# Optimization experiments

Measured on AMD Instinct MI355X. Metric: run time of the kernel, lower is better.

Reference implementation:

```python
import jax, jax.numpy as jnp
import numpy as np

B, TQ, TI, TT = 8, 256, 256, 256
H, NH, F, E = 1024, 16, 4096, 8
HD = H // NH
EPS = 1e-5


def _ln(x, g, b):
    m = x.mean(-1, keepdims=True)
    v = ((x - m) ** 2).mean(-1, keepdims=True)
    return (x - m) / jnp.sqrt(v + EPS) * g + b


def _mha(q, k, v, in_w, in_b, out_w, out_b):
    # torch nn.MultiheadAttention: packed in_proj [3H,H], out_proj [H,H]
    wq, wk, wv = jnp.split(in_w, 3, axis=0)
    bq, bk, bv = jnp.split(in_b, 3, axis=0)
    Bq, Tq, _ = q.shape
    Tk = k.shape[1]
    qh = (q @ wq.T + bq).reshape(Bq, Tq, NH, HD)
    kh = (k @ wk.T + bk).reshape(Bq, Tk, NH, HD)
    vh = (v @ wv.T + bv).reshape(Bq, Tk, NH, HD)
    scores = jnp.einsum('bqhd,bkhd->bhqk', qh, kh) / jnp.sqrt(jnp.float32(HD))
    attn = jax.nn.softmax(scores, axis=-1)
    out = jnp.einsum('bhqk,bkhd->bqhd', attn, vh).reshape(Bq, Tq, H)
    return out @ out_w.T + out_b


def _moe(x, w1, b1, w2, b2, probs):
    # dense all-expert FFN: GELU(x W1 + b1) W2 + b2, mixed by router probs
    h = jax.nn.gelu(jnp.einsum('bth,ehf->btef', x, w1) + b1, approximate=False)
    o = jnp.einsum('btef,efh->bteh', h, w2) + b2
    return (o * probs[..., None]).sum(axis=-2)


def setup_inputs() -> dict:
    key = jax.random.key(0)
    ks = jax.random.split(key, 24)
    s = 0.02
    d = {}
    d['query_tokens'] = jax.random.normal(ks[0], (B, TQ, H), jnp.float32)
    d['image_tokens'] = jax.random.normal(ks[1], (B, TI, H), jnp.float32)
    d['text_context'] = jax.random.normal(ks[2], (B, TT, H), jnp.float32)
    d['sa_in_w'] = jax.random.normal(ks[3], (3 * H, H), jnp.float32) * s
    d['sa_in_b'] = jnp.zeros((3 * H,), jnp.float32)
    d['sa_out_w'] = jax.random.normal(ks[4], (H, H), jnp.float32) * s
    d['sa_out_b'] = jnp.zeros((H,), jnp.float32)
    d['ca_in_w'] = jax.random.normal(ks[5], (3 * H, H), jnp.float32) * s
    d['ca_in_b'] = jnp.zeros((3 * H,), jnp.float32)
    d['ca_out_w'] = jax.random.normal(ks[6], (H, H), jnp.float32) * s
    d['ca_out_b'] = jnp.zeros((H,), jnp.float32)
    d['img_gate_w'] = jax.random.normal(ks[7], (E, 2 * H), jnp.float32) * s
    d['img_gate_b'] = jnp.zeros((E,), jnp.float32)
    d['txt_gate_w'] = jax.random.normal(ks[8], (E, 2 * H), jnp.float32) * s
    d['txt_gate_b'] = jnp.zeros((E,), jnp.float32)
    d['lnq_g'] = jnp.ones((H,), jnp.float32)
    d['lnq_b'] = jnp.zeros((H,), jnp.float32)
    d['lnc_g'] = jnp.ones((H,), jnp.float32)
    d['lnc_b'] = jnp.zeros((H,), jnp.float32)
    d['lnf_g'] = jnp.ones((H,), jnp.float32)
    d['lnf_b'] = jnp.zeros((H,), jnp.float32)
    d['ew1'] = jax.random.normal(ks[9], (E, H, F), jnp.float32) * s
    d['eb1'] = jnp.zeros((E, F), jnp.float32)
    d['ew2'] = jax.random.normal(ks[10], (E, F, H), jnp.float32) * s
    d['eb2'] = jnp.zeros((E, H), jnp.float32)
    return d


def reference(query_tokens, image_tokens, text_context,
              sa_in_w, sa_in_b, sa_out_w, sa_out_b,
              ca_in_w, ca_in_b, ca_out_w, ca_out_b,
              img_gate_w, img_gate_b, txt_gate_w, txt_gate_b,
              lnq_g, lnq_b, lnc_g, lnc_b, lnf_g, lnf_b,
              ew1, eb1, ew2, eb2):
    # self-attention on query stream (dropout is identity in eval)
    q_norm = _ln(query_tokens, lnq_g, lnq_b)
    query_tokens = query_tokens + _mha(q_norm, q_norm, q_norm, sa_in_w, sa_in_b, sa_out_w, sa_out_b)
    # cross-attention query -> image tokens
    cross_norm = _ln(query_tokens, lnc_g, lnc_b)
    query_tokens = query_tokens + _mha(cross_norm, image_tokens, image_tokens, ca_in_w, ca_in_b, ca_out_w, ca_out_b)
    # gating contexts
    image_ctx = image_tokens.mean(axis=1, keepdims=True)   # [B,1,H]
    text_ctx = text_context.mean(axis=1, keepdims=True)    # [B,1,H]
    img_gate_in = jnp.concatenate([image_tokens, jnp.broadcast_to(text_ctx, image_tokens.shape)], axis=-1)
    txt_gate_in = jnp.concatenate([query_tokens, jnp.broadcast_to(image_ctx, query_tokens.shape)], axis=-1)
    temp = jnp.maximum(jnp.float32(1.0), 0.001)  # router temperature buffer = 1.0
    image_probs = jax.nn.softmax((img_gate_in @ img_gate_w.T + img_gate_b) / temp, axis=-1)
    text_probs = jax.nn.softmax((txt_gate_in @ txt_gate_w.T + txt_gate_b) / temp, axis=-1)
    # dense MoE (ep_group is None -> all experts evaluated, mixed by full softmax)
    q_ffn = _ln(query_tokens, lnf_g, lnf_b)
    query_tokens = query_tokens + _moe(q_ffn, ew1, eb1, ew2, eb2, text_probs)
    image_tokens = image_tokens + _moe(image_tokens, ew1, eb1, ew2, eb2, image_probs)
    return query_tokens, image_tokens
```

## Files before the change

kernel.cpp:

```cpp
#include <hip/hip_runtime.h>
#include <math.h>

typedef unsigned short u16;
typedef __bf16 bf16x8 __attribute__((ext_vector_type(8)));
typedef float  f32x4  __attribute__((ext_vector_type(4)));
typedef unsigned short u16x8 __attribute__((ext_vector_type(8)));
typedef unsigned short u16x4 __attribute__((ext_vector_type(4)));

union B8 { u16x8 u; bf16x8 b; };

__device__ __forceinline__ u16 f2bf(float x) {
  unsigned int u = __float_as_uint(x);
  unsigned int r = (u + 0x7fffu + ((u >> 16) & 1u)) >> 16;
  return (u16)r;
}
__device__ __forceinline__ float bf2f(u16 h) {
  return __uint_as_float(((unsigned int)h) << 16);
}

__device__ __forceinline__ void gload16(const void* g, void* l) {
  __builtin_amdgcn_global_load_lds(
      (const __attribute__((address_space(1))) unsigned int*)g,
      (__attribute__((address_space(3))) unsigned int*)l, 16, 0, 0);
}

__global__ __launch_bounds__(256) void cast_kernel(const float* __restrict__ in,
                                                   u16* __restrict__ out, int n4) {
  int i = blockIdx.x * 256 + threadIdx.x;
  if (i >= n4) return;
  f32x4 v = *(const f32x4*)(in + (size_t)i * 4);
  u16x4 o;
  o[0] = f2bf(v[0]); o[1] = f2bf(v[1]); o[2] = f2bf(v[2]); o[3] = f2bf(v[3]);
  *(u16x4*)(out + (size_t)i * 4) = o;
}

__global__ void transpose_cast_kernel(const float* __restrict__ in, u16* __restrict__ out,
                                      int R, int C) {
  __shared__ float tile[32][33];
  int z = blockIdx.z;
  int r0 = blockIdx.y * 32, c0 = blockIdx.x * 32;
  const float* ip = in + (size_t)z * R * C;
  u16* op = out + (size_t)z * R * C;
  int tx = threadIdx.x, ty = threadIdx.y;
  #pragma unroll
  for (int i = 0; i < 32; i += 8)
    tile[ty + i][tx] = ip[(size_t)(r0 + ty + i) * C + c0 + tx];
  __syncthreads();
  #pragma unroll
  for (int i = 0; i < 32; i += 8)
    op[(size_t)(c0 + ty + i) * R + r0 + tx] = f2bf(tile[tx][ty + i]);
}

__global__ __launch_bounds__(256) void ln_kernel(const float* __restrict__ in,
                                                 const float* __restrict__ g,
                                                 const float* __restrict__ bt,
                                                 u16* __restrict__ out) {
  __shared__ float red[4];
  int row = blockIdx.x;
  int t = threadIdx.x;
  int lane = t & 63, wid = t >> 6;
  f32x4 x = *(const f32x4*)(in + (size_t)row * 1024 + t * 4);
  float s = x[0] + x[1] + x[2] + x[3];
  #pragma unroll
  for (int o = 32; o > 0; o >>= 1) s += __shfl_down(s, o, 64);
  if (lane == 0) red[wid] = s;
  __syncthreads();
  float mean = (red[0] + red[1] + red[2] + red[3]) * (1.0f / 1024.0f);
  __syncthreads();
  float d0 = x[0] - mean, d1 = x[1] - mean, d2 = x[2] - mean, d3 = x[3] - mean;
  float s2 = d0 * d0 + d1 * d1 + d2 * d2 + d3 * d3;
  #pragma unroll
  for (int o = 32; o > 0; o >>= 1) s2 += __shfl_down(s2, o, 64);
  if (lane == 0) red[wid] = s2;
  __syncthreads();
  float var = (red[0] + red[1] + red[2] + red[3]) * (1.0f / 1024.0f);
  float rstd = rsqrtf(var + 1e-5f);
  f32x4 gg = *(const f32x4*)(g + t * 4);
  f32x4 bb = *(const f32x4*)(bt + t * 4);
  u16x4 o;
  o[0] = f2bf(d0 * rstd * gg[0] + bb[0]);
  o[1] = f2bf(d1 * rstd * gg[1] + bb[1]);
  o[2] = f2bf(d2 * rstd * gg[2] + bb[2]);
  o[3] = f2bf(d3 * rstd * gg[3] + bb[3]);
  *(u16x4*)(out + (size_t)row * 1024 + t * 4) = o;
}

__device__ __forceinline__ float gelu_f(float x) {
  float y = 0.79788456080286536f * (x + 0.044715f * x * x * x);
  return x - __fdividef(x, __expf(2.0f * y) + 1.0f);
}

#define SRC_COL(t) ((((t) & 3) ^ (((t) >> 3) & 3)) * 8)

template <int MODE, int ZB, int CHUNK>
__global__ __launch_bounds__(256, 3) void gemm_bt(const u16* __restrict__ A,
                                                  const u16* __restrict__ B,
                                                  const float* __restrict__ bias,
                                                  const float* __restrict__ extra,
                                                  void* __restrict__ out,
                                                  int M, int N, int K, int expertBase,
                                                  int kChunk, size_t saz, size_t sbz,
                                                  int sbiasz, size_t soutz) {
  __shared__ u16 sm[24576];
  const int tid = threadIdx.x;
  const int lane = tid & 63;
  const int wid = tid >> 6;
  const int wr = wid >> 1, wc = wid & 1;
  const int l15 = lane & 15;
  const int kg = lane >> 4;
  const int kgr8 = (kg ^ ((lane >> 1) & 3)) * 8;
  const int z = blockIdx.z;

  if (ZB) { A += (size_t)z * saz; B += (size_t)z * sbz; bias += z * sbiasz; }
  const int kOff = ZB ? 0 : z * kChunk;
  const bool z0 = ZB ? true : (z == 0);
  const int expert = expertBase + (ZB ? z : 0);

  const int gx = gridDim.x, gy = gridDim.y;
  const int bid = blockIdx.y * gx + blockIdx.x;
  const int xcd = bid & 7;
  const int idx = bid >> 3;
  int m0, n0;
  if constexpr (CHUNK == 0) {
    const int nwg = gx * gy;
    const int swz = xcd * (nwg >> 3) + idx;
    m0 = (swz / gx) * 128;
    n0 = (swz % gx) * 128;
  } else {
    const int hy = gy >> 2, hx = gx >> 1;
    const int cy = xcd >> 1, cx = xcd & 1;
    const int mloc = idx % hy;
    const int nloc = idx / hy;
    m0 = (cy * hy + mloc) * 128;
    n0 = (cx * hx + nloc) * 128;
  }

  f32x4 acc[4][4];
  #pragma unroll
  for (int i = 0; i < 4; i++)
    #pragma unroll
    for (int j = 0; j < 4; j++) acc[i][j] = f32x4{0.f, 0.f, 0.f, 0.f};

  const int sc = SRC_COL(tid);
  const u16* ga = A + (size_t)(m0 + (tid >> 2)) * K + sc + kOff;
  const u16* gb = B + (size_t)(n0 + (tid >> 2)) * K + sc + kOff;
  const size_t rowskip = (size_t)64 * K;

#define STG(b, kt)                                                  \
  do {                                                              \
    u16* d = sm + (b) * 8192 + wid * 512;                           \
    gload16(ga + (kt), d);                                          \
    gload16(ga + rowskip + (kt), d + 2048);                         \
    gload16(gb + (kt), d + 4096);                                   \
    gload16(gb + rowskip + (kt), d + 6144);                         \
  } while (0)

  const int NT = kChunk >> 5;
  STG(0, 0); STG(1, 32);
  int buf = 0;
  for (int t = 0; t < NT; ++t) {
    if (t + 1 < NT) asm volatile("s_waitcnt vmcnt(4)" ::: "memory");
    else            asm volatile("s_waitcnt vmcnt(0)" ::: "memory");
    __builtin_amdgcn_s_barrier();
    if (t + 2 < NT) {
      int nb = buf + 2; if (nb >= 3) nb -= 3;
      STG(nb, (t + 2) * 32);
    }
    __builtin_amdgcn_sched_barrier(0);
    __builtin_amdgcn_s_setprio(1);
    const u16* base = sm + buf * 8192;
    B8 af[4], bfr[4];
    #pragma unroll
    for (int i = 0; i < 4; i++) {
      af[i].u  = *(const u16x8*)(base + (wr * 64 + l15 + i * 16) * 32 + kgr8);
      bfr[i].u = *(const u16x8*)(base + 4096 + (wc * 64 + l15 + i * 16) * 32 + kgr8);
    }
    #pragma unroll
    for (int i = 0; i < 4; i++)
      #pragma unroll
      for (int j = 0; j < 4; j++)
        acc[i][j] = __builtin_amdgcn_mfma_f32_16x16x32_bf16(af[i].b, bfr[j].b, acc[i][j], 0, 0, 0);
    __builtin_amdgcn_s_setprio(0);
    if (++buf >= 3) buf = 0;
  }
#undef STG

  const int orow0 = m0 + wr * 64 + (lane >> 4) * 4;
  const int ocol0 = n0 + wc * 64 + l15;

  if constexpr (MODE == 0 || MODE == 2) {
    u16* outp = (u16*)out + (ZB ? (size_t)z * soutz : 0);
    __builtin_amdgcn_s_barrier();
    u16* rp = sm + wid * 1152;
    const int mrow0 = m0 + wr * 64;
    const int cbase = n0 + wc * 64;
    #pragma unroll
    for (int i = 0; i < 4; i++) {
      #pragma unroll
      for (int j = 0; j < 4; j++) {
        const float bb = bias[cbase + j * 16 + l15];
        #pragma unroll
        for (int p = 0; p < 4; p++) {
          float vb = acc[i][j][p] + bb;
          if constexpr (MODE == 2) vb = gelu_f(vb);
          rp[((lane >> 4) * 4 + p) * 72 + j * 16 + l15] = f2bf(vb);
        }
      }
      asm volatile("s_waitcnt lgkmcnt(0)" ::: "memory");
      #pragma unroll
      for (int rr = 0; rr < 4; rr++) {
        const int r16 = rr * 4 + (lane >> 4);
        u16x4 v4 = *(const u16x4*)&rp[r16 * 72 + l15 * 4];
        *(u16x4*)(outp + (size_t)(mrow0 + i * 16 + r16) * N + cbase + l15 * 4) = v4;
      }
      asm volatile("s_waitcnt lgkmcnt(0)" ::: "memory");
    }
  } else {
    float* outp = (float*)out + (ZB ? (size_t)z * soutz : 0);
    #pragma unroll
    for (int i = 0; i < 4; i++) {
      float pr_[4];
      if constexpr (MODE == 3) {
        #pragma unroll
        for (int p = 0; p < 4; p++)
          pr_[p] = extra[(size_t)(orow0 + i * 16 + p) * 8 + expert];
      }
      #pragma unroll
      for (int j = 0; j < 4; j++) {
        const int gcol = ocol0 + j * 16;
        const float bb = bias[gcol];
        #pragma unroll
        for (int p = 0; p < 4; p++) {
          const int grow = orow0 + i * 16 + p;
          const size_t off = (size_t)grow * N + gcol;
          if constexpr (MODE == 1) {
            atomicAdd(&outp[off], acc[i][j][p] + (z0 ? bb + extra[off] : 0.f));
          } else {
            atomicAdd(&outp[off], pr_[p] * (acc[i][j][p] + bb));
          }
        }
      }
    }
  }
}

__global__ __launch_bounds__(256) void attn_mfma(const u16* __restrict__ qb, int qs,
                                                 const u16* __restrict__ kb_, int ks,
                                                 const u16* __restrict__ vb, int vs,
                                                 u16* __restrict__ outp) {
  __shared__ u16 Ks[64][72];
  __shared__ u16 Vt[64][72];
  __shared__ u16 Pl[4][64][72];
  const int t = threadIdx.x;
  const int lane = t & 63;
  const int w = t >> 6;
  const int b = blockIdx.x >> 4;
  const int h = blockIdx.x & 15;
  const int lr = lane & 15;
  const int kg = lane >> 4;
  const size_t qrow0 = (size_t)b * 256 + w * 64;

  B8 qf[4][2];
  #pragma unroll
  for (int i = 0; i < 4; i++)
    #pragma unroll
    for (int kk = 0; kk < 2; kk++)
      qf[i][kk].u = *(const u16x8*)(qb + (qrow0 + i * 16 + lr) * qs + h * 64 + kk * 32 + kg * 8);

  f32x4 ao[4][4];
  float m_[4][4], l_[4][4];
  #pragma unroll
  for (int i = 0; i < 4; i++)
    #pragma unroll
    for (int n = 0; n < 4; n++) ao[i][n] = f32x4{0.f, 0.f, 0.f, 0.f};
  #pragma unroll
  for (int i = 0; i < 4; i++)
    #pragma unroll
    for (int p = 0; p < 4; p++) { m_[i][p] = -1e30f; l_[i][p] = 0.f; }

  for (int jt = 0; jt < 4; ++jt) {
    __syncthreads();
    {
      int r = t >> 2, c = (t & 3) * 16;
      const u16* src = kb_ + ((size_t)b * 256 + jt * 64 + r) * ks + h * 64 + c;
      *(u16x8*)&Ks[r][c] = *(const u16x8*)src;
      *(u16x8*)&Ks[r][c + 8] = *(const u16x8*)(src + 8);
      int jj = t & 63;
      const u16* vsrc = vb + ((size_t)b * 256 + jt * 64 + jj) * vs + h * 64 + w * 16;
      u16x8 v0 = *(const u16x8*)vsrc;
      u16x8 v1 = *(const u16x8*)(vsrc + 8);
      #pragma unroll
      for (int d = 0; d < 8; d++) Vt[w * 16 + d][jj] = v0[d];
      #pragma unroll
      for (int d = 0; d < 8; d++) Vt[w * 16 + 8 + d][jj] = v1[d];
    }
    __syncthreads();

    B8 kf[2][4];
    #pragma unroll
    for (int kk = 0; kk < 2; kk++)
      #pragma unroll
      for (int n = 0; n < 4; n++)
        kf[kk][n].u = *(const u16x8*)&Ks[n * 16 + lr][kk * 32 + kg * 8];

    #pragma unroll
    for (int i = 0; i < 4; i++) {
      f32x4 s[4];
      #pragma unroll
      for (int n = 0; n < 4; n++) s[n] = f32x4{0.f, 0.f, 0.f, 0.f};
      #pragma unroll
      for (int kk = 0; kk < 2; kk++)
        #pragma unroll
        for (int n = 0; n < 4; n++)
          s[n] = __builtin_amdgcn_mfma_f32_16x16x32_bf16(qf[i][kk].b, kf[kk][n].b, s[n], 0, 0, 0);
      #pragma unroll
      for (int p = 0; p < 4; p++) {
        float pm = fmaxf(fmaxf(s[0][p], s[1][p]), fmaxf(s[2][p], s[3][p])) * 0.125f;
        #pragma unroll
        for (int mk = 1; mk < 16; mk <<= 1) pm = fmaxf(pm, __shfl_xor(pm, mk, 16));
        float mn = fmaxf(m_[i][p], pm);
        float scl = __expf(m_[i][p] - mn);
        m_[i][p] = mn;
        float rs = 0.f;
        #pragma unroll
        for (int n = 0; n < 4; n++) {
          float e = __expf(s[n][p] * 0.125f - mn);
          Pl[w][i * 16 + kg * 4 + p][n * 16 + lr] = f2bf(e);
          rs += e;
        }
        #pragma unroll
        for (int mk = 1; mk < 16; mk <<= 1) rs += __shfl_xor(rs, mk, 16);
        l_[i][p] = l_[i][p] * scl + rs;
        #pragma unroll
        for (int n2 = 0; n2 < 4; n2++) ao[i][n2][p] *= scl;
      }
    }

    B8 vf[2][4];
    #pragma unroll
    for (int kk = 0; kk < 2; kk++)
      #pragma unroll
      for (int n2 = 0; n2 < 4; n2++)
        vf[kk][n2].u = *(const u16x8*)&Vt[n2 * 16 + lr][kk * 32 + kg * 8];
    #pragma unroll
    for (int i = 0; i < 4; i++) {
      #pragma unroll
      for (int kk = 0; kk < 2; kk++) {
        B8 pa;
        pa.u = *(const u16x8*)&Pl[w][i * 16 + lr][kk * 32 + kg * 8];
        #pragma unroll
        for (int n2 = 0; n2 < 4; n2++)
          ao[i][n2] = __builtin_amdgcn_mfma_f32_16x16x32_bf16(pa.b, vf[kk][n2].b, ao[i][n2], 0, 0, 0);
      }
    }
  }

  #pragma unroll
  for (int i = 0; i < 4; i++) {
    #pragma unroll
    for (int p = 0; p < 4; p++) {
      const float inv = 1.0f / l_[i][p];
      const size_t row = qrow0 + i * 16 + kg * 4 + p;
      #pragma unroll
      for (int n2 = 0; n2 < 4; n2++)
        outp[row * 1024 + h * 64 + n2 * 16 + lr] = f2bf(ao[i][n2][p] * inv);
    }
  }
}

__global__ __launch_bounds__(256) void mean2_kernel(const float* __restrict__ in,
                                                    float* __restrict__ out) {
  __shared__ float part[128];
  const int blk = blockIdx.x;
  const int b = blk >> 3, ch = blk & 7;
  const int t = threadIdx.x;
  const int col = ch * 128 + (t & 127);
  const int half = t >> 7;
  const float* p = in + (size_t)b * 262144 + (size_t)half * 131072 + col;
  float s = 0.f;
  for (int r = 0; r < 128; r++) s += p[(size_t)r * 1024];
  if (half) part[t & 127] = s;
  __syncthreads();
  if (!half) out[b * 1024 + col] = (s + part[t & 127]) * (1.0f / 256.0f);
}

__global__ __launch_bounds__(256) void gate_kernel(const float* __restrict__ x,
                                                   const float* __restrict__ ctx,
                                                   const float* __restrict__ gw,
                                                   const float* __restrict__ gb,
                                                   float* __restrict__ probs, int rowoff) {
  __shared__ float lg[8];
  const int tok = blockIdx.x;
  const int b = tok >> 8;
  const int t = threadIdx.x;
  const int e = t >> 5, sl = t & 31;
  const float* xr = x + (size_t)tok * 1024;
  const float* cr = ctx + (size_t)b * 1024;
  const float* wrow = gw + (size_t)e * 2048;
  float s = 0.f;
  for (int c = sl; c < 1024; c += 32) s += xr[c] * wrow[c] + cr[c] * wrow[1024 + c];
  #pragma unroll
  for (int o = 16; o > 0; o >>= 1) s += __shfl_down(s, o, 32);
  if (sl == 0) lg[e] = s + gb[e];
  __syncthreads();
  if (t == 0) {
    float mx = lg[0];
    #pragma unroll
    for (int i = 1; i < 8; i++) mx = fmaxf(mx, lg[i]);
    float ex[8], sum = 0.f;
    #pragma unroll
    for (int i = 0; i < 8; i++) { ex[i] = expf(lg[i] - mx); sum += ex[i]; }
    float inv = 1.0f / sum;
    #pragma unroll
    for (int i = 0; i < 8; i++) probs[(size_t)(rowoff + tok) * 8 + i] = ex[i] * inv;
  }
}

__global__ __launch_bounds__(256) void final_add_kernel(const float* __restrict__ q3,
                                                        const float* __restrict__ img,
                                                        const float* __restrict__ moe,
                                                        float* __restrict__ out) {
  size_t i = (size_t)blockIdx.x * 256 + threadIdx.x;
  f32x4 m4 = *(const f32x4*)(moe + i * 4);
  f32x4 a4 = (i < 524288) ? *(const f32x4*)(q3 + i * 4)
                          : *(const f32x4*)(img + (i - 524288) * 4);
  f32x4 r;
  r[0] = a4[0] + m4[0]; r[1] = a4[1] + m4[1]; r[2] = a4[2] + m4[2]; r[3] = a4[3] + m4[3];
  *(f32x4*)(out + i * 4) = r;
}

extern "C" void kernel_launch(void* const* d_in, const int* in_sizes, int n_in,
                              void* d_out, int out_size, void* d_ws, size_t ws_size,
                              hipStream_t stream) {
  const float* query_in = (const float*)d_in[0];
  const float* image_in = (const float*)d_in[1];
  const float* text_in  = (const float*)d_in[2];
  const float* sa_in_w  = (const float*)d_in[3];
  const float* sa_in_b  = (const float*)d_in[4];
  const float* sa_out_w = (const float*)d_in[5];
  const float* sa_out_b = (const float*)d_in[6];
  const float* ca_in_w  = (const float*)d_in[7];
  const float* ca_in_b  = (const float*)d_in[8];
  const float* ca_out_w = (const float*)d_in[9];
  const float* ca_out_b = (const float*)d_in[10];
  const float* img_gate_w = (const float*)d_in[11];
  const float* img_gate_b = (const float*)d_in[12];
  const float* txt_gate_w = (const float*)d_in[13];
  const float* txt_gate_b = (const float*)d_in[14];
  const float* lnq_g = (const float*)d_in[15];
  const float* lnq_b = (const float*)d_in[16];
  const float* lnc_g = (const float*)d_in[17];
  const float* lnc_b = (const float*)d_in[18];
  const float* lnf_g = (const float*)d_in[19];
  const float* lnf_b = (const float*)d_in[20];
  const float* ew1 = (const float*)d_in[21];
  const float* eb1 = (const float*)d_in[22];
  const float* ew2 = (const float*)d_in[23];
  const float* eb2 = (const float*)d_in[24];

  char* base = (char*)d_ws;
  size_t off = 0;
  auto alloc = [&](size_t bytes) -> char* {
    char* p = base + off;
    off += (bytes + 255) & ~(size_t)255;
    return p;
  };

  u16* wsa_in  = (u16*)alloc((size_t)3072 * 1024 * 2);
  u16* wsa_out = (u16*)alloc((size_t)1024 * 1024 * 2);
  u16* wca_in  = (u16*)alloc((size_t)3072 * 1024 * 2);
  u16* wca_out = (u16*)alloc((size_t)1024 * 1024 * 2);
  u16* w1T = (u16*)alloc((size_t)8 * 4096 * 1024 * 2);
  u16* w2T = (u16*)alloc((size_t)8 * 4096 * 1024 * 2);
  char* big = alloc((size_t)67108864);
  float* q3 = (float*)alloc((size_t)2048 * 1024 * 4);
  u16* xmoe = (u16*)alloc((size_t)4096 * 1024 * 2);
  float* moeac = (float*)alloc((size_t)4096 * 1024 * 4);
  float* probs = (float*)alloc((size_t)4096 * 8 * 4);
  float* ctx = (float*)alloc((size_t)2 * 8192 * 4);

  u16* qn      = (u16*)big;
  u16* qkv     = (u16*)(big + 4194304);
  u16* attn_o  = (u16*)(big + 16777216);
  float* q2    = (float*)(big + 20971520);
  u16* cnorm   = (u16*)(big + 29360128);
  u16* qca     = (u16*)(big + 33554432);
  u16* kvca    = (u16*)(big + 37748736);
  u16* h1p     = (u16*)big;
  u16* img_bf  = xmoe + (size_t)2048 * 1024;

  cast_kernel<<<3072, 256, 0, stream>>>(sa_in_w, wsa_in, 786432);
  cast_kernel<<<1024, 256, 0, stream>>>(sa_out_w, wsa_out, 262144);
  cast_kernel<<<3072, 256, 0, stream>>>(ca_in_w, wca_in, 786432);
  cast_kernel<<<1024, 256, 0, stream>>>(ca_out_w, wca_out, 262144);
  transpose_cast_kernel<<<dim3(128, 32, 8), dim3(32, 8), 0, stream>>>(ew1, w1T, 1024, 4096);
  transpose_cast_kernel<<<dim3(32, 128, 8), dim3(32, 8), 0, stream>>>(ew2, w2T, 4096, 1024);
  cast_kernel<<<2048, 256, 0, stream>>>(image_in, img_bf, 524288);

  ln_kernel<<<2048, 256, 0, stream>>>(query_in, lnq_g, lnq_b, qn);
  gemm_bt<0, 0, 0><<<dim3(24, 16), 256, 0, stream>>>(qn, wsa_in, sa_in_b, nullptr, qkv,
                                                     2048, 3072, 1024, 0, 1024, 0, 0, 0, 0);
  attn_mfma<<<128, 256, 0, stream>>>(qkv, 3072, qkv + 1024, 3072, qkv + 2048, 3072, attn_o);
  hipMemsetAsync(q2, 0, (size_t)2048 * 1024 * 4, stream);
  gemm_bt<1, 0, 0><<<dim3(8, 16, 2), 256, 0, stream>>>(attn_o, wsa_out, sa_out_b, query_in, q2,
                                                       2048, 1024, 1024, 0, 512, 0, 0, 0, 0);

  ln_kernel<<<2048, 256, 0, stream>>>(q2, lnc_g, lnc_b, cnorm);
  gemm_bt<0, 0, 0><<<dim3(8, 16), 256, 0, stream>>>(cnorm, wca_in, ca_in_b, nullptr, qca,
                                                    2048, 1024, 1024, 0, 1024, 0, 0, 0, 0);
  gemm_bt<0, 0, 0><<<dim3(16, 16), 256, 0, stream>>>(img_bf, wca_in + (size_t)1024 * 1024,
                                                     ca_in_b + 1024, nullptr, kvca,
                                                     2048, 2048, 1024, 0, 1024, 0, 0, 0, 0);
  attn_mfma<<<128, 256, 0, stream>>>(qca, 1024, kvca, 2048, kvca + 1024, 2048, attn_o);
  hipMemsetAsync(q3, 0, (size_t)2048 * 1024 * 4, stream);
  gemm_bt<1, 0, 0><<<dim3(8, 16, 2), 256, 0, stream>>>(attn_o, wca_out, ca_out_b, q2, q3,
                                                       2048, 1024, 1024, 0, 512, 0, 0, 0, 0);

  mean2_kernel<<<64, 256, 0, stream>>>(image_in, ctx);
  mean2_kernel<<<64, 256, 0, stream>>>(text_in, ctx + 8192);
  gate_kernel<<<2048, 256, 0, stream>>>(q3, ctx, txt_gate_w, txt_gate_b, probs, 0);
  gate_kernel<<<2048, 256, 0, stream>>>(image_in, ctx + 8192, img_gate_w, img_gate_b, probs, 2048);

  ln_kernel<<<2048, 256, 0, stream>>>(q3, lnf_g, lnf_b, xmoe);
  hipMemsetAsync(moeac, 0, (size_t)4096 * 1024 * 4, stream);
  for (int e0 = 0; e0 < 8; e0 += 2) {
    gemm_bt<2, 1, 2><<<dim3(32, 32, 2), 256, 0, stream>>>(
        xmoe, w1T + (size_t)e0 * 4194304, eb1 + (size_t)e0 * 4096, nullptr, h1p,
        4096, 4096, 1024, e0, 1024,
         0,  4194304,  4096,  16777216);
    gemm_bt<3, 1, 0><<<dim3(8, 32, 2), 256, 0, stream>>>(
        h1p, w2T + (size_t)e0 * 4194304, eb2 + (size_t)e0 * 1024, probs, moeac,
        4096, 1024, 4096, e0, 4096,
         16777216,  4194304,  1024,  0);
  }

  final_add_kernel<<<4096, 256, 0, stream>>>(q3, image_in, moeac, (float*)d_out);
}
```

Before: 1.132 ms.

## Use 256x128 tiles for MoE W1 GEMM and split-K the W2 GEMM

Adds a dedicated gemm_w1 kernel with 256x128 output tiles (8x4 MFMA accumulators per wave, 3-stage LDS pipeline) for the expert up-projection. The larger tile raises arithmetic intensity per B-tile load, at the cost of more registers and lower occupancy (launch bounds 2). The down-projection GEMM gets a new ZB==2 mode that splits K in two across the z dimension, doubling the grid for better CU fill. Only the first K-half adds the bias; the price is twice as many atomic adds into the accumulator.

After: 1.163 ms. 2.8% more time.

```diff
diff --git a/kernel.cpp b/kernel.cpp
--- a/kernel.cpp
+++ b/kernel.cpp
@@ -111,10 +111,11 @@
   const int kgr8 = (kg ^ ((lane >> 1) & 3)) * 8;
   const int z = blockIdx.z;
 
-  if (ZB) { A += (size_t)z * saz; B += (size_t)z * sbz; bias += z * sbiasz; }
-  const int kOff = ZB ? 0 : z * kChunk;
-  const bool z0 = ZB ? true : (z == 0);
-  const int expert = expertBase + (ZB ? z : 0);
+  const int ze = (ZB == 2) ? (z >> 1) : z;
+  if (ZB) { A += (size_t)ze * saz; B += (size_t)ze * sbz; bias += ze * sbiasz; }
+  const int kOff = (ZB == 0) ? z * kChunk : (ZB == 2 ? (z & 1) * kChunk : 0);
+  const bool z0 = (ZB == 0) ? (z == 0) : (ZB == 1 ? true : ((z & 1) == 0));
+  const int expert = expertBase + (ZB ? ze : 0);
 
   const int gx = gridDim.x, gy = gridDim.y;
   const int bid = blockIdx.y * gx + blockIdx.x;
@@ -189,7 +190,7 @@
   const int ocol0 = n0 + wc * 64 + l15;
 
   if constexpr (MODE == 0 || MODE == 2) {
-    u16* outp = (u16*)out + (ZB ? (size_t)z * soutz : 0);
+    u16* outp = (u16*)out + (ZB ? (size_t)ze * soutz : 0);
     __builtin_amdgcn_s_barrier();
     u16* rp = sm + wid * 1152;
     const int mrow0 = m0 + wr * 64;
@@ -216,7 +217,7 @@
       asm volatile("s_waitcnt lgkmcnt(0)" ::: "memory");
     }
   } else {
-    float* outp = (float*)out + (ZB ? (size_t)z * soutz : 0);
+    float* outp = (float*)out + (ZB ? (size_t)ze * soutz : 0);
     #pragma unroll
     for (int i = 0; i < 4; i++) {
       float pr_[4];
@@ -236,11 +237,117 @@
           if constexpr (MODE == 1) {
             atomicAdd(&outp[off], acc[i][j][p] + (z0 ? bb + extra[off] : 0.f));
           } else {
-            atomicAdd(&outp[off], pr_[p] * (acc[i][j][p] + bb));
+            atomicAdd(&outp[off], pr_[p] * (acc[i][j][p] + (z0 ? bb : 0.f)));
           }
         }
       }
     }
+  }
+}
+
+__global__ __launch_bounds__(256, 2) void gemm_w1(const u16* __restrict__ A,
+                                                  const u16* __restrict__ B,
+                                                  const float* __restrict__ bias,
+                                                  u16* __restrict__ out,
+                                                  int N, int K,
+                                                  size_t sbz, int sbiasz, size_t soutz) {
+  __shared__ u16 sm[36864];
+  const int tid = threadIdx.x;
+  const int lane = tid & 63;
+  const int wid = tid >> 6;
+  const int wr = wid >> 1, wc = wid & 1;
+  const int l15 = lane & 15;
+  const int kg = lane >> 4;
+  const int kgr8 = (kg ^ ((lane >> 1) & 3)) * 8;
+  const int z = blockIdx.z;
+  B += (size_t)z * sbz; bias += z * sbiasz;
+  u16* outp = out + (size_t)z * soutz;
+
+  const int gx = gridDim.x, gy = gridDim.y;
+  const int bid = blockIdx.y * gx + blockIdx.x;
+  const int xcd = bid & 7;
+  const int idx = bid >> 3;
+  const int hy = gy >> 2, hx = gx >> 1;
+  const int cy = xcd >> 1, cx = xcd & 1;
+  const int m0 = (cy * hy + idx % hy) * 256;
+  const int n0 = (cx * hx + idx / hy) * 128;
+
+  f32x4 acc[8][4];
+  #pragma unroll
+  for (int i = 0; i < 8; i++)
+    #pragma unroll
+    for (int j = 0; j < 4; j++) acc[i][j] = f32x4{0.f, 0.f, 0.f, 0.f};
+
+  const int sc = SRC_COL(tid);
+  const u16* ga = A + (size_t)(m0 + (tid >> 2)) * K + sc;
+  const u16* gb = B + (size_t)(n0 + (tid >> 2)) * K + sc;
+  const size_t r64 = (size_t)64 * K;
+
+#define STGW(b, kt)                                                 \
+  do {                                                              \
+    u16* d = sm + (b) * 12288 + wid * 512;                          \
+    gload16(ga + (kt), d);                                          \
+    gload16(ga + r64 + (kt), d + 2048);                             \
+    gload16(ga + 2 * r64 + (kt), d + 4096);                         \
+    gload16(ga + 3 * r64 + (kt), d + 6144);                         \
+    gload16(gb + (kt), d + 8192);                                   \
+    gload16(gb + r64 + (kt), d + 10240);                            \
+  } while (0)
+
+  const int NT = K >> 5;
+  STGW(0, 0); STGW(1, 32);
+  int buf = 0;
+  for (int t = 0; t < NT; ++t) {
+    if (t + 1 < NT) asm volatile("s_waitcnt vmcnt(6)" ::: "memory");
+    else            asm volatile("s_waitcnt vmcnt(0)" ::: "memory");
+    __builtin_amdgcn_s_barrier();
+    if (t + 2 < NT) {
+      int nb = buf + 2; if (nb >= 3) nb -= 3;
+      STGW(nb, (t + 2) * 32);
+    }
+    __builtin_amdgcn_sched_barrier(0);
+    __builtin_amdgcn_s_setprio(1);
+    const u16* base = sm + buf * 12288;
+    B8 af[8], bfr[4];
+    #pragma unroll
+    for (int j = 0; j < 4; j++)
+      bfr[j].u = *(const u16x8*)(base + 8192 + (wc * 64 + j * 16 + l15) * 32 + kgr8);
+    #pragma unroll
+    for (int i = 0; i < 8; i++)
+      af[i].u = *(const u16x8*)(base + (wr * 128 + i * 16 + l15) * 32 + kgr8);
+    #pragma unroll
+    for (int i = 0; i < 8; i++)
+      #pragma unroll
+      for (int j = 0; j < 4; j++)
+        acc[i][j] = __builtin_amdgcn_mfma_f32_16x16x32_bf16(af[i].b, bfr[j].b, acc[i][j], 0, 0, 0);
+    __builtin_amdgcn_s_setprio(0);
+    if (++buf >= 3) buf = 0;
+  }
+#undef STGW
+
+  __builtin_amdgcn_s_barrier();
+  u16* rp = sm + wid * 1152;
+  const int mrow0 = m0 + wr * 128;
+  const int cbase = n0 + wc * 64;
+  #pragma unroll
+  for (int i = 0; i < 8; i++) {
+    #pragma unroll
+    for (int j = 0; j < 4; j++) {
+      const float bb = bias[cbase + j * 16 + l15];
+      #pragma unroll
+      for (int p = 0; p < 4; p++) {
+        float vb = gelu_f(acc[i][j][p] + bb);
+        rp[((lane >> 4) * 4 + p) * 72 + j * 16 + l15] = f2bf(vb);
+      }
+    }
+    asm volatile("s_waitcnt lgkmcnt(0)" ::: "memory");
+    #pragma unroll
+    for (int rr = 0; rr < 4; rr++) {
+      const int r16 = rr * 4 + (lane >> 4);
+      u16x4 v4 = *(const u16x4*)&rp[r16 * 72 + l15 * 4];
+      *(u16x4*)(outp + (size_t)(mrow0 + i * 16 + r16) * N + cbase + l15 * 4) = v4;
+    }
+    asm volatile("s_waitcnt lgkmcnt(0)" ::: "memory");
   }
 }
 
@@ -524,13 +631,12 @@
   ln_kernel<<<2048, 256, 0, stream>>>(q3, lnf_g, lnf_b, xmoe);
   hipMemsetAsync(moeac, 0, (size_t)4096 * 1024 * 4, stream);
   for (int e0 = 0; e0 < 8; e0 += 2) {
-    gemm_bt<2, 1, 2><<<dim3(32, 32, 2), 256, 0, stream>>>(
-        xmoe, w1T + (size_t)e0 * 4194304, eb1 + (size_t)e0 * 4096, nullptr, h1p,
-        4096, 4096, 1024, e0, 1024,
-         0,  4194304,  4096,  16777216);
-    gemm_bt<3, 1, 0><<<dim3(8, 32, 2), 256, 0, stream>>>(
+    gemm_w1<<<dim3(32, 16, 2), 256, 0, stream>>>(
+        xmoe, w1T + (size_t)e0 * 4194304, eb1 + (size_t)e0 * 4096, h1p,
+        4096, 1024,  4194304,  4096,  16777216);
+    gemm_bt<3, 2, 0><<<dim3(8, 32, 4), 256, 0, stream>>>(
         h1p, w2T + (size_t)e0 * 4194304, eb2 + (size_t)e0 * 1024, probs, moeac,
-        4096, 1024, 4096, e0, 4096,
+        4096, 1024, 4096, e0, 2048,
          16777216,  4194304,  1024,  0);
   }
 
```
